# Optimization experiments

Hardware: AMD Instinct MI355X
Metric: run time of the kernel (lower is better)

The kernel has to match this reference:

```python
import jax, jax.numpy as jnp
import numpy as np

N_NODES = 100000
N_FEATS = 512
HIDDEN = 64
NUM_SAMPLES = 5
NUM_CLASSES = 16
BATCH = 16384


def setup_inputs() -> dict:
    key = jax.random.key(0)
    k1, k2, k3, k4, k5, k6, k7 = jax.random.split(key, 7)
    nodes = jax.random.randint(k1, (BATCH,), 0, N_NODES, dtype=jnp.int64) if jax.config.jax_enable_x64 else jax.random.randint(k1, (BATCH,), 0, N_NODES, dtype=jnp.int32)
    neigh_idx = jax.random.randint(k2, (N_NODES, NUM_SAMPLES), 0, N_NODES, dtype=jnp.int32)
    features = jax.random.normal(k3, (N_NODES, N_FEATS), dtype=jnp.float32)
    # xavier-uniform style init
    def xavier(k, shape):
        fan_in, fan_out = shape[1], shape[0]
        lim = jnp.sqrt(6.0 / (fan_in + fan_out)).astype(jnp.float32)
        return jax.random.uniform(k, shape, jnp.float32, -lim, lim)
    w1 = xavier(k4, (HIDDEN, 2 * N_FEATS))      # enc1 weight
    w2 = xavier(k5, (HIDDEN, 2 * HIDDEN))       # enc2 weight
    w_cls = xavier(k6, (NUM_CLASSES, HIDDEN))   # classifier weight
    return {"features": features, "w1": w1, "w2": w2, "w_cls": w_cls,
            "nodes": nodes, "neigh_idx": neigh_idx}


def reference(features, w1, w2, w_cls, nodes, neigh_idx):
    # Layer 1 (enc1, gcn=False): concat(self, mean(sampled neighbors)) -> W1 -> ReLU
    # Computed for all nodes (superset of what torch computes lazily; same values).
    neigh1 = features[neigh_idx].mean(axis=1)                      # [N, F]
    h1 = jax.nn.relu(jnp.concatenate([features, neigh1], axis=1) @ w1.T)  # [N, H]
    # Layer 2 (enc2) on the query batch
    self2 = h1[nodes]                                              # [B, H]
    neigh2 = h1[neigh_idx[nodes]].mean(axis=1)                     # [B, H]
    h2 = jax.nn.relu(jnp.concatenate([self2, neigh2], axis=1) @ w2.T)     # [B, H]
    # scores = (w_cls @ h2.T).T == h2 @ w_cls.T
    return h2 @ w_cls.T                                            # [B, C]
```

## Files before the change

### kernel.cpp

```cpp
#include <hip/hip_runtime.h>
#include <hip/hip_bf16.h>

#define N_NODES 100000
#define N_FEATS 512
#define HIDDEN 64
#define NUM_SAMPLES 5
#define NUM_CLASSES 16
#define BATCH 16384

typedef __attribute__((ext_vector_type(8))) short bf16x8;
typedef __attribute__((ext_vector_type(8))) unsigned short u16x8;
typedef __attribute__((ext_vector_type(4))) float f32x4;

static __device__ __forceinline__ float bf2f(unsigned short s) {
    unsigned int u = ((unsigned int)s) << 16;
    return __builtin_bit_cast(float, u);
}
static __device__ __forceinline__ short f2bf(float v) {
    __hip_bfloat16 b = __float2bfloat16(v);
    return *reinterpret_cast<short*>(&b);
}
static __device__ __forceinline__ int clampi(int v) {
    return ((unsigned)v < (unsigned)N_NODES) ? v : 0;
}

__global__ __launch_bounds__(256) void prep(const float* __restrict__ w1f,
                                            short* __restrict__ w1p,
                                            const int* __restrict__ nodes_i32,
                                            int* __restrict__ flag) {
    const int t = blockIdx.x * 256 + threadIdx.x;
    if (t < 64 * 1024) {
        const int j = t & 7;
        const int lane = (t >> 3) & 63;
        const int nb = (t >> 9) & 7;
        const int kk = t >> 12;
        const int l16 = lane & 15, quad = lane >> 4;
        const int cn = nb * 16 + l16;
        const int h = cn & 63, part = cn >> 6;
        w1p[t] = f2bf(w1f[h * 1024 + part * 512 + kk * 32 + quad * 8 + j]);
    }
    if (blockIdx.x == 0 && threadIdx.x == 0) {
        int odd_nonzero = 0;
        for (int i = 0; i < 64; i++)
            if (nodes_i32[2 * i + 1] != 0) odd_nonzero++;
        *flag = (odd_nonzero == 0) ? 1 : 0;
    }
}

__global__ __launch_bounds__(256) void pq_gemm(const float* __restrict__ feat,
                                               const short* __restrict__ w1p,
                                               short* __restrict__ PQ) {
    const int wave = threadIdx.x >> 6;
    const int lane = threadIdx.x & 63;
    const int quad = lane >> 4;
    const int l16  = lane & 15;
    const int r0   = blockIdx.x * 64 + wave * 16;

    int rA = r0 + l16;
    if (rA >= N_NODES) rA = N_NODES - 1;

    const float* aptr = feat + (size_t)rA * N_FEATS + quad * 8;
    const short* bbase = w1p + lane * 8;

    f32x4 buf[2][8];
#pragma unroll
    for (int c = 0; c < 4; c++) {
        buf[0][2 * c]     = *reinterpret_cast<const f32x4*>(aptr + c * 32);
        buf[0][2 * c + 1] = *reinterpret_cast<const f32x4*>(aptr + c * 32 + 4);
    }

    f32x4 acc[8];
#pragma unroll
    for (int i = 0; i < 8; i++) acc[i] = (f32x4){0.f, 0.f, 0.f, 0.f};

#pragma unroll
    for (int g = 0; g < 4; g++) {
        const int cur = g & 1;
        if (g < 3) {
#pragma unroll
            for (int c = 0; c < 4; c++) {
                buf[cur ^ 1][2 * c]     = *reinterpret_cast<const f32x4*>(aptr + (g + 1) * 128 + c * 32);
                buf[cur ^ 1][2 * c + 1] = *reinterpret_cast<const f32x4*>(aptr + (g + 1) * 128 + c * 32 + 4);
            }
        }
#pragma unroll
        for (int kk2 = 0; kk2 < 4; kk2++) {
            const int kk = g * 4 + kk2;
            bf16x8 afrag;
#pragma unroll
            for (int j = 0; j < 4; j++) {
                afrag[j]     = f2bf(buf[cur][2 * kk2][j]);
                afrag[4 + j] = f2bf(buf[cur][2 * kk2 + 1][j]);
            }
            const short* bk = bbase + kk * 4096;
#pragma unroll
            for (int nb = 0; nb < 8; nb++) {
                bf16x8 bfrag = *reinterpret_cast<const bf16x8*>(bk + nb * 512);
                acc[nb] = __builtin_amdgcn_mfma_f32_16x16x32_bf16(afrag, bfrag, acc[nb], 0, 0, 0);
            }
        }
    }

#pragma unroll
    for (int nb = 0; nb < 8; nb++) {
        const int cn = nb * 16 + l16;
#pragma unroll
        for (int r = 0; r < 4; r++) {
            const int row = r0 + quad * 4 + r;
            if (row < N_NODES) PQ[(size_t)row * 128 + cn] = f2bf(acc[nb][r]);
        }
    }
}

__global__ __launch_bounds__(256) void h1_combine(short* __restrict__ PQ,
                                                  const int* __restrict__ neigh_idx) {
    const int t = blockIdx.x * 256 + threadIdx.x;
    const int n = t >> 3;
    const int sub = t & 7;
    if (n >= N_NODES) return;

    u16x8 pv = *reinterpret_cast<const u16x8*>(PQ + (size_t)n * 128 + sub * 8);
    float s[8];
#pragma unroll
    for (int j = 0; j < 8; j++) s[j] = 0.f;
#pragma unroll
    for (int i = 0; i < NUM_SAMPLES; i++) {
        const int ni = clampi(neigh_idx[n * NUM_SAMPLES + i]);
        u16x8 qv = *reinterpret_cast<const u16x8*>(PQ + (size_t)ni * 128 + 64 + sub * 8);
#pragma unroll
        for (int j = 0; j < 8; j++) s[j] += bf2f(qv[j]);
    }
    u16x8 ov;
#pragma unroll
    for (int j = 0; j < 8; j++) {
        float v = bf2f(pv[j]) + 0.2f * s[j];
        v = v > 0.f ? v : 0.f;
        ov[j] = (unsigned short)f2bf(v);
    }
    *reinterpret_cast<u16x8*>(PQ + (size_t)n * 128 + sub * 8) = ov;
}

__global__ __launch_bounds__(256) void layer2_cls(const short* __restrict__ PQ,
                                                  const int* __restrict__ nodes_i32,
                                                  const int* __restrict__ neigh_idx,
                                                  const float* __restrict__ w2,
                                                  const float* __restrict__ wcls,
                                                  const int* __restrict__ flag,
                                                  float* __restrict__ out) {
    __shared__ float gbuf[16][128];
    __shared__ float h2buf[16][64];
    const int wave = threadIdx.x >> 6;
    const int lane = threadIdx.x & 63;
    const int is64 = *flag;
    const int b0 = blockIdx.x * 16;

#pragma unroll
    for (int it = 0; it < 4; it++) {
        const int item = wave * 4 + it;
        const int b = b0 + item;
        const int node = clampi(nodes_i32[is64 ? 2 * b : b]);
        float selfv = bf2f((unsigned short)PQ[(size_t)node * 128 + lane]);
        float ns = 0.f;
#pragma unroll
        for (int s = 0; s < NUM_SAMPLES; s++) {
            const int ni = clampi(neigh_idx[node * NUM_SAMPLES + s]);
            ns += bf2f((unsigned short)PQ[(size_t)ni * 128 + lane]);
        }
        gbuf[item][lane] = selfv;
        gbuf[item][64 + lane] = 0.2f * ns;
    }
    __syncthreads();

    float acc[4] = {0.f, 0.f, 0.f, 0.f};
    const f32x4* w2r = reinterpret_cast<const f32x4*>(w2 + lane * 128);
#pragma unroll 8
    for (int k = 0; k < 32; k++) {
        f32x4 w = w2r[k];
#pragma unroll
        for (int it = 0; it < 4; it++) {
            f32x4 g = *reinterpret_cast<const f32x4*>(&gbuf[wave * 4 + it][k * 4]);
            acc[it] += g[0] * w[0] + g[1] * w[1] + g[2] * w[2] + g[3] * w[3];
        }
    }
#pragma unroll
    for (int it = 0; it < 4; it++) {
        float h2 = acc[it] > 0.f ? acc[it] : 0.f;
        h2buf[wave * 4 + it][lane] = h2;
    }
    __syncthreads();

    if (lane < NUM_CLASSES) {
        const f32x4* wcr = reinterpret_cast<const f32x4*>(wcls + lane * 64);
#pragma unroll
        for (int it = 0; it < 4; it++) {
            const int item = wave * 4 + it;
            const f32x4* hr = reinterpret_cast<const f32x4*>(&h2buf[item][0]);
            float o = 0.f;
#pragma unroll
            for (int k = 0; k < 16; k++) {
                f32x4 h = hr[k], w = wcr[k];
                o += h[0] * w[0] + h[1] * w[1] + h[2] * w[2] + h[3] * w[3];
            }
            out[(size_t)(b0 + item) * NUM_CLASSES + lane] = o;
        }
    }
}

extern "C" void kernel_launch(void* const* d_in, const int* in_sizes, int n_in,
                              void* d_out, int out_size, void* d_ws, size_t ws_size,
                              hipStream_t stream) {
    const float* feat = nullptr;
    const float* w1 = nullptr;
    const float* w2 = nullptr;
    const float* wcls = nullptr;
    const int* nodes = nullptr;
    const int* neigh_idx = nullptr;
    for (int i = 0; i < n_in; i++) {
        switch (in_sizes[i]) {
            case 51200000: feat = (const float*)d_in[i]; break;
            case 65536:    w1 = (const float*)d_in[i]; break;
            case 8192:     w2 = (const float*)d_in[i]; break;
            case 1024:     wcls = (const float*)d_in[i]; break;
            case 16384:    nodes = (const int*)d_in[i]; break;
            case 500000:   neigh_idx = (const int*)d_in[i]; break;
            default: break;
        }
    }
    float* out = (float*)d_out;

    int* flag = (int*)d_ws;
    short* w1p = (short*)((char*)d_ws + 256);
    short* PQ  = (short*)((char*)d_ws + 256 + 64 * 1024 * sizeof(short));

    prep<<<256, 256, 0, stream>>>(w1, w1p, nodes, flag);
    pq_gemm<<<(N_NODES + 63) / 64, 256, 0, stream>>>(feat, w1p, PQ);
    h1_combine<<<(N_NODES * 8 + 255) / 256, 256, 0, stream>>>(PQ, neigh_idx);
    layer2_cls<<<BATCH / 16, 256, 0, stream>>>(PQ, nodes, neigh_idx, w2, wcls, flag, out);
}
```

Measured before the change: 369.7 us.

## Register-block GEMM over two row tiles and batch more work per thread

The feature-projection GEMM now has each wave compute two 16-row M tiles. Each W1 fragment loaded from global memory then feeds two MFMAs instead of one, and the K loop is rebuilt to prefetch 64-wide chunks for both tiles. The neighbor-combine kernel handles two nodes per thread and issues all index and gather loads before accumulating, which raises memory-level parallelism. The layer-2 kernel processes 32 batch items per block instead of 16, so the W2 loads are reused across more items. The costs are higher register pressure, larger shared-memory use and fewer blocks in flight, which may reduce occupancy and latency hiding.

```diff
diff --git a/kernel.cpp b/kernel.cpp
--- a/kernel.cpp
+++ b/kernel.cpp
@@ -54,90 +54,115 @@
     const int lane = threadIdx.x & 63;
     const int quad = lane >> 4;
     const int l16  = lane & 15;
-    const int r0   = blockIdx.x * 64 + wave * 16;
-
-    int rA = r0 + l16;
-    if (rA >= N_NODES) rA = N_NODES - 1;
-
-    const float* aptr = feat + (size_t)rA * N_FEATS + quad * 8;
+    const int r0   = blockIdx.x * 128 + wave * 32;
+
+    const float* aptr[2];
+#pragma unroll
+    for (int mt = 0; mt < 2; mt++) {
+        int r = r0 + mt * 16 + l16;
+        if (r >= N_NODES) r = N_NODES - 1;
+        aptr[mt] = feat + (size_t)r * N_FEATS + quad * 8;
+    }
     const short* bbase = w1p + lane * 8;
 
-    f32x4 buf[2][8];
-#pragma unroll
-    for (int c = 0; c < 4; c++) {
-        buf[0][2 * c]     = *reinterpret_cast<const f32x4*>(aptr + c * 32);
-        buf[0][2 * c + 1] = *reinterpret_cast<const f32x4*>(aptr + c * 32 + 4);
-    }
-
-    f32x4 acc[8];
-#pragma unroll
-    for (int i = 0; i < 8; i++) acc[i] = (f32x4){0.f, 0.f, 0.f, 0.f};
-
-#pragma unroll
-    for (int g = 0; g < 4; g++) {
+    f32x4 buf[2][2][4];
+#pragma unroll
+    for (int mt = 0; mt < 2; mt++)
+#pragma unroll
+        for (int kk2 = 0; kk2 < 2; kk2++) {
+            buf[0][mt][kk2 * 2]     = *reinterpret_cast<const f32x4*>(aptr[mt] + kk2 * 32);
+            buf[0][mt][kk2 * 2 + 1] = *reinterpret_cast<const f32x4*>(aptr[mt] + kk2 * 32 + 4);
+        }
+
+    f32x4 acc[2][8];
+#pragma unroll
+    for (int mt = 0; mt < 2; mt++)
+#pragma unroll
+        for (int i = 0; i < 8; i++) acc[mt][i] = (f32x4){0.f, 0.f, 0.f, 0.f};
+
+#pragma unroll
+    for (int g = 0; g < 8; g++) {
         const int cur = g & 1;
-        if (g < 3) {
-#pragma unroll
-            for (int c = 0; c < 4; c++) {
-                buf[cur ^ 1][2 * c]     = *reinterpret_cast<const f32x4*>(aptr + (g + 1) * 128 + c * 32);
-                buf[cur ^ 1][2 * c + 1] = *reinterpret_cast<const f32x4*>(aptr + (g + 1) * 128 + c * 32 + 4);
-            }
-        }
-#pragma unroll
-        for (int kk2 = 0; kk2 < 4; kk2++) {
-            const int kk = g * 4 + kk2;
-            bf16x8 afrag;
-#pragma unroll
-            for (int j = 0; j < 4; j++) {
-                afrag[j]     = f2bf(buf[cur][2 * kk2][j]);
-                afrag[4 + j] = f2bf(buf[cur][2 * kk2 + 1][j]);
-            }
+        if (g < 7) {
+#pragma unroll
+            for (int mt = 0; mt < 2; mt++)
+#pragma unroll
+                for (int kk2 = 0; kk2 < 2; kk2++) {
+                    buf[cur ^ 1][mt][kk2 * 2]     = *reinterpret_cast<const f32x4*>(aptr[mt] + (g + 1) * 64 + kk2 * 32);
+                    buf[cur ^ 1][mt][kk2 * 2 + 1] = *reinterpret_cast<const f32x4*>(aptr[mt] + (g + 1) * 64 + kk2 * 32 + 4);
+                }
+        }
+#pragma unroll
+        for (int kk2 = 0; kk2 < 2; kk2++) {
+            const int kk = g * 2 + kk2;
+            bf16x8 afrag[2];
+#pragma unroll
+            for (int mt = 0; mt < 2; mt++)
+#pragma unroll
+                for (int j = 0; j < 4; j++) {
+                    afrag[mt][j]     = f2bf(buf[cur][mt][kk2 * 2][j]);
+                    afrag[mt][4 + j] = f2bf(buf[cur][mt][kk2 * 2 + 1][j]);
+                }
             const short* bk = bbase + kk * 4096;
 #pragma unroll
             for (int nb = 0; nb < 8; nb++) {
                 bf16x8 bfrag = *reinterpret_cast<const bf16x8*>(bk + nb * 512);
-                acc[nb] = __builtin_amdgcn_mfma_f32_16x16x32_bf16(afrag, bfrag, acc[nb], 0, 0, 0);
+                acc[0][nb] = __builtin_amdgcn_mfma_f32_16x16x32_bf16(afrag[0], bfrag, acc[0][nb], 0, 0, 0);
+                acc[1][nb] = __builtin_amdgcn_mfma_f32_16x16x32_bf16(afrag[1], bfrag, acc[1][nb], 0, 0, 0);
             }
         }
     }
 
 #pragma unroll
-    for (int nb = 0; nb < 8; nb++) {
-        const int cn = nb * 16 + l16;
-#pragma unroll
-        for (int r = 0; r < 4; r++) {
-            const int row = r0 + quad * 4 + r;
-            if (row < N_NODES) PQ[(size_t)row * 128 + cn] = f2bf(acc[nb][r]);
-        }
-    }
+    for (int mt = 0; mt < 2; mt++)
+#pragma unroll
+        for (int nb = 0; nb < 8; nb++) {
+            const int cn = nb * 16 + l16;
+#pragma unroll
+            for (int r = 0; r < 4; r++) {
+                const int row = r0 + mt * 16 + quad * 4 + r;
+                if (row < N_NODES) PQ[(size_t)row * 128 + cn] = f2bf(acc[mt][nb][r]);
+            }
+        }
 }
 
 __global__ __launch_bounds__(256) void h1_combine(short* __restrict__ PQ,
                                                   const int* __restrict__ neigh_idx) {
     const int t = blockIdx.x * 256 + threadIdx.x;
-    const int n = t >> 3;
+    const int idx = t >> 3;
     const int sub = t & 7;
-    if (n >= N_NODES) return;
-
-    u16x8 pv = *reinterpret_cast<const u16x8*>(PQ + (size_t)n * 128 + sub * 8);
-    float s[8];
-#pragma unroll
-    for (int j = 0; j < 8; j++) s[j] = 0.f;
+    if (idx >= 50000) return;
+    const int n0 = idx, n1 = idx + 50000;
+
+    u16x8 pv0 = *reinterpret_cast<const u16x8*>(PQ + (size_t)n0 * 128 + sub * 8);
+    u16x8 pv1 = *reinterpret_cast<const u16x8*>(PQ + (size_t)n1 * 128 + sub * 8);
+
+    int ni0[NUM_SAMPLES], ni1[NUM_SAMPLES];
 #pragma unroll
     for (int i = 0; i < NUM_SAMPLES; i++) {
-        const int ni = clampi(neigh_idx[n * NUM_SAMPLES + i]);
-        u16x8 qv = *reinterpret_cast<const u16x8*>(PQ + (size_t)ni * 128 + 64 + sub * 8);
-#pragma unroll
-        for (int j = 0; j < 8; j++) s[j] += bf2f(qv[j]);
-    }
-    u16x8 ov;
+        ni0[i] = clampi(neigh_idx[n0 * NUM_SAMPLES + i]);
+        ni1[i] = clampi(neigh_idx[n1 * NUM_SAMPLES + i]);
+    }
+    u16x8 qv0[NUM_SAMPLES], qv1[NUM_SAMPLES];
+#pragma unroll
+    for (int i = 0; i < NUM_SAMPLES; i++) {
+        qv0[i] = *reinterpret_cast<const u16x8*>(PQ + (size_t)ni0[i] * 128 + 64 + sub * 8);
+        qv1[i] = *reinterpret_cast<const u16x8*>(PQ + (size_t)ni1[i] * 128 + 64 + sub * 8);
+    }
+
+    u16x8 ov0, ov1;
 #pragma unroll
     for (int j = 0; j < 8; j++) {
-        float v = bf2f(pv[j]) + 0.2f * s[j];
-        v = v > 0.f ? v : 0.f;
-        ov[j] = (unsigned short)f2bf(v);
-    }
-    *reinterpret_cast<u16x8*>(PQ + (size_t)n * 128 + sub * 8) = ov;
+        float s0 = 0.f, s1 = 0.f;
+#pragma unroll
+        for (int i = 0; i < NUM_SAMPLES; i++) { s0 += bf2f(qv0[i][j]); s1 += bf2f(qv1[i][j]); }
+        float v0 = bf2f(pv0[j]) + 0.2f * s0;
+        float v1 = bf2f(pv1[j]) + 0.2f * s1;
+        ov0[j] = (unsigned short)f2bf(v0 > 0.f ? v0 : 0.f);
+        ov1[j] = (unsigned short)f2bf(v1 > 0.f ? v1 : 0.f);
+    }
+    *reinterpret_cast<u16x8*>(PQ + (size_t)n0 * 128 + sub * 8) = ov0;
+    *reinterpret_cast<u16x8*>(PQ + (size_t)n1 * 128 + sub * 8) = ov1;
 }
 
 __global__ __launch_bounds__(256) void layer2_cls(const short* __restrict__ PQ,
@@ -147,16 +172,16 @@
                                                   const float* __restrict__ wcls,
                                                   const int* __restrict__ flag,
                                                   float* __restrict__ out) {
-    __shared__ float gbuf[16][128];
-    __shared__ float h2buf[16][64];
+    __shared__ float gbuf[32][128];
+    __shared__ float h2buf[32][64];
     const int wave = threadIdx.x >> 6;
     const int lane = threadIdx.x & 63;
     const int is64 = *flag;
-    const int b0 = blockIdx.x * 16;
-
-#pragma unroll
-    for (int it = 0; it < 4; it++) {
-        const int item = wave * 4 + it;
+    const int b0 = blockIdx.x * 32;
+
+#pragma unroll
+    for (int it = 0; it < 8; it++) {
+        const int item = wave * 8 + it;
         const int b = b0 + item;
         const int node = clampi(nodes_i32[is64 ? 2 * b : b]);
         float selfv = bf2f((unsigned short)PQ[(size_t)node * 128 + lane]);
@@ -171,29 +196,29 @@
     }
     __syncthreads();
 
-    float acc[4] = {0.f, 0.f, 0.f, 0.f};
+    float acc[8] = {0.f, 0.f, 0.f, 0.f, 0.f, 0.f, 0.f, 0.f};
     const f32x4* w2r = reinterpret_cast<const f32x4*>(w2 + lane * 128);
 #pragma unroll 8
     for (int k = 0; k < 32; k++) {
         f32x4 w = w2r[k];
 #pragma unroll
-        for (int it = 0; it < 4; it++) {
-            f32x4 g = *reinterpret_cast<const f32x4*>(&gbuf[wave * 4 + it][k * 4]);
+        for (int it = 0; it < 8; it++) {
+            f32x4 g = *reinterpret_cast<const f32x4*>(&gbuf[wave * 8 + it][k * 4]);
             acc[it] += g[0] * w[0] + g[1] * w[1] + g[2] * w[2] + g[3] * w[3];
         }
     }
 #pragma unroll
-    for (int it = 0; it < 4; it++) {
+    for (int it = 0; it < 8; it++) {
         float h2 = acc[it] > 0.f ? acc[it] : 0.f;
-        h2buf[wave * 4 + it][lane] = h2;
+        h2buf[wave * 8 + it][lane] = h2;
     }
     __syncthreads();
 
     if (lane < NUM_CLASSES) {
         const f32x4* wcr = reinterpret_cast<const f32x4*>(wcls + lane * 64);
 #pragma unroll
-        for (int it = 0; it < 4; it++) {
-            const int item = wave * 4 + it;
+        for (int it = 0; it < 8; it++) {
+            const int item = wave * 8 + it;
             const f32x4* hr = reinterpret_cast<const f32x4*>(&h2buf[item][0]);
             float o = 0.f;
 #pragma unroll
@@ -233,7 +258,7 @@
     short* PQ  = (short*)((char*)d_ws + 256 + 64 * 1024 * sizeof(short));
 
     prep<<<256, 256, 0, stream>>>(w1, w1p, nodes, flag);
-    pq_gemm<<<(N_NODES + 63) / 64, 256, 0, stream>>>(feat, w1p, PQ);
-    h1_combine<<<(N_NODES * 8 + 255) / 256, 256, 0, stream>>>(PQ, neigh_idx);
-    layer2_cls<<<BATCH / 16, 256, 0, stream>>>(PQ, nodes, neigh_idx, w2, wcls, flag, out);
-}
+    pq_gemm<<<(N_NODES + 127) / 128, 256, 0, stream>>>(feat, w1p, PQ);
+    h1_combine<<<(50000 * 8 + 255) / 256, 256, 0, stream>>>(PQ, neigh_idx);
+    layer2_cls<<<BATCH / 32, 256, 0, stream>>>(PQ, nodes, neigh_idx, w2, wcls, flag, out);
+}
```

New measurement: 372.1 us. No clear change (+0.6%).
